# Optimization experiments

Measured on AMD Instinct MI355X. Metric: run time of the kernel, lower is better.

The kernel has to match this reference:

```python
import jax, jax.numpy as jnp
import numpy as np

B, D, C, H, L = 32768, 64, 64, 1024, 6
EPS = 1e-5
NIN = (D - D // 2) + C  # unchanged half + cond = 96
SPLIT = D // 2          # 32


def setup_inputs() -> dict:
    key = jax.random.key(0)
    ks = jax.random.split(key, 12)
    s = 0.05
    return {
        "z": jax.random.normal(ks[0], (B, D), jnp.float32),
        "cond": jax.random.normal(ks[1], (B, C), jnp.float32),
        "W1": jax.random.normal(ks[2], (L, NIN, H), jnp.float32) * s,
        "b1": jax.random.normal(ks[3], (L, H), jnp.float32) * s,
        "W2": jax.random.normal(ks[4], (L, H, H), jnp.float32) * s,
        "b2": jax.random.normal(ks[5], (L, H), jnp.float32) * s,
        "Ws": jax.random.normal(ks[6], (L, H, SPLIT), jnp.float32) * s,
        "bs": jax.random.normal(ks[7], (L, SPLIT), jnp.float32) * s,
        "Wt": jax.random.normal(ks[8], (L, H, SPLIT), jnp.float32) * s,
        "bt": jax.random.normal(ks[9], (L, SPLIT), jnp.float32) * s,
        "bn_w": 1.0 + 0.1 * jax.random.normal(ks[10], (L, D), jnp.float32),
        "bn_b": 0.1 * jax.random.normal(ks[11], (L, D), jnp.float32),
    }


def reference(z, cond, W1, b1, W2, b2, Ws, bs, Wt, bt, bn_w, bn_b):
    x = z
    log_det = jnp.zeros((z.shape[0],), z.dtype)
    for i in range(L):
        # 'even' mask keeps even indices on even layers, odd indices otherwise
        if i % 2 == 0:
            keep, chg = np.arange(0, D, 2), np.arange(1, D, 2)
        else:
            keep, chg = np.arange(1, D, 2), np.arange(0, D, 2)
        # 2-layer MLP on [x_keep, cond]
        h = jax.nn.relu(jnp.concatenate([x[:, keep], cond], axis=1) @ W1[i] + b1[i])
        h = jax.nn.relu(h @ W2[i] + b2[i])
        log_s = jnp.tanh(h @ Ws[i] + bs[i])          # (B, SPLIT)
        t = h @ Wt[i] + bt[i]                         # (B, SPLIT)
        x2t = x[:, chg] * jnp.exp(log_s) + t
        x = jnp.zeros_like(x).at[:, keep].set(x[:, keep]).at[:, chg].set(x2t)
        log_det = log_det + log_s.sum(axis=1)
        # BatchNorm1d, training mode: batch mean / biased variance, eps=1e-5
        mean = x.mean(axis=0)
        var = x.var(axis=0)
        x = (x - mean) * jax.lax.rsqrt(var + EPS) * bn_w[i] + bn_b[i]
        log_det = log_det + jnp.log(jnp.abs(bn_w[i])).sum()
    return x, log_det
```

## Files before the change

kernel.cpp:

```cpp
#include <hip/hip_runtime.h>
#include <math.h>

#define BB 32768
#define DD 64
#define CC 64
#define HH 1024
#define LL 6
#define SPLIT 32
#define NIN 96
#define EPSV 1e-5f

typedef short short8 __attribute__((ext_vector_type(8)));
typedef float f32x4 __attribute__((ext_vector_type(4)));
typedef unsigned short u16;

__device__ __forceinline__ u16 f2bf(float f) {
    union { float f; unsigned int u; } c; c.f = f;
    unsigned int u = c.u + 0x7FFFu + ((c.u >> 16) & 1u);
    return (u16)(u >> 16);
}

__device__ __forceinline__ void gl_lds16(const u16* g, u16* l) {
    __builtin_amdgcn_global_load_lds(
        (const __attribute__((address_space(1))) unsigned int*)g,
        (__attribute__((address_space(3))) unsigned int*)l, 16, 0, 0);
}

__global__ void transpose_cvt_kernel(const float* __restrict__ src, u16* __restrict__ dst,
                                     int R, int C, int Rpad,
                                     long long sstride, long long dstride)
{
    __shared__ float tile[32][33];
    const float* s = src + (size_t)blockIdx.z * sstride;
    u16* d = dst + (size_t)blockIdx.z * dstride;
    int r0 = blockIdx.x * 32, c0 = blockIdx.y * 32;
    int tc = threadIdx.x & 31, tr = threadIdx.x >> 5;
#pragma unroll
    for (int i = 0; i < 4; ++i) {
        int r = r0 + tr + i * 8;
        tile[tr + i * 8][tc] = (r < R) ? s[(size_t)r * C + c0 + tc] : 0.f;
    }
    __syncthreads();
#pragma unroll
    for (int i = 0; i < 4; ++i) {
        int cc = tr + i * 8;
        d[(size_t)(c0 + cc) * Rpad + r0 + tc] = f2bf(tile[tc][cc]);
    }
}

__global__ __launch_bounds__(256)
void init_ain_cond_kernel(const float* __restrict__ cond, u16* __restrict__ Ain)
{
    int t = blockIdx.x * 256 + threadIdx.x;
    int c = t % 96, r = t / 96;
    Ain[(size_t)r * 128 + 32 + c] = (c < CC) ? f2bf(cond[(size_t)r * CC + c]) : (u16)0;
}

__global__ __launch_bounds__(256)
void build_keep_kernel(const float* __restrict__ x, u16* __restrict__ Ain, int keep_off)
{
    int t = blockIdx.x * 256 + threadIdx.x;
    int c = t & 31, r = t >> 5;
    Ain[(size_t)r * 128 + c] = f2bf(x[(size_t)r * DD + 2 * c + keep_off]);
}

__global__ __launch_bounds__(512, 4)
void gemm_tiled(const u16* __restrict__ A,
                const u16* __restrict__ Bt,
                const float* __restrict__ bias,
                u16* __restrict__ Cc,
                int K)
{
    __shared__ u16 sA[2][8 * 512];
    __shared__ u16 sB[2][16 * 512];

    const int t = threadIdx.x;
    const int w = t >> 6, lane = t & 63;
    const int lane16 = lane & 15, quad = lane >> 4;
    const int wm = w >> 2, wn = w & 3;

    int id = blockIdx.x;
    int nby = gridDim.x >> 2;
    int xcd = id & 7, slot = id >> 3;
    int bx = slot & 3, byq = slot >> 2;
    int by = xcd * (nby >> 3) + byq;
    const int bm = by * 128, bn = bx * 256;

    const int niter = K >> 5;

    auto stage = [&](int it, int buf) {
        int k0 = it * 32;
#pragma unroll
        for (int e3 = 0; e3 < 3; ++e3) {
            int e = w + e3 * 8;
            if (e < 8) {
                const u16* g = A + (size_t)(bm + e * 16 + lane16) * K + k0 + quad * 8;
                gl_lds16(g, &sA[buf][e * 512]);
            } else {
                int j = e - 8;
                const u16* g = Bt + (size_t)(bn + j * 16 + lane16) * K + k0 + quad * 8;
                gl_lds16(g, &sB[buf][j * 512]);
            }
        }
    };

    f32x4 acc[4][4];
#pragma unroll
    for (int a = 0; a < 4; ++a)
#pragma unroll
        for (int b = 0; b < 4; ++b) acc[a][b] = (f32x4){0.f, 0.f, 0.f, 0.f};

    stage(0, 0);
    for (int it = 0; it < niter; ++it) {
        const int buf = it & 1;
        __syncthreads();
        if (it + 1 < niter) stage(it + 1, buf ^ 1);
        short8 af[4], bf[4];
#pragma unroll
        for (int a = 0; a < 4; ++a)
            af[a] = *(const short8*)(&sA[buf][(wm * 4 + a) * 512 + lane * 8]);
#pragma unroll
        for (int b = 0; b < 4; ++b)
            bf[b] = *(const short8*)(&sB[buf][(wn * 4 + b) * 512 + lane * 8]);
#pragma unroll
        for (int a = 0; a < 4; ++a)
#pragma unroll
            for (int b = 0; b < 4; ++b)
                acc[a][b] = __builtin_amdgcn_mfma_f32_16x16x32_bf16(af[a], bf[b], acc[a][b], 0, 0, 0);
    }
    __syncthreads();

    constexpr int ES = 72;
    float bv[4];
#pragma unroll
    for (int b = 0; b < 4; ++b) bv[b] = bias[bn + wn * 64 + b * 16 + lane16];
    u16* scr = ((u16*)sB) + w * (16 * ES);
#pragma unroll
    for (int a = 0; a < 4; ++a) {
#pragma unroll
        for (int b = 0; b < 4; ++b)
#pragma unroll
            for (int r = 0; r < 4; ++r) {
                float v = fmaxf(acc[a][b][r] + bv[b], 0.f);
                scr[(quad * 4 + r) * ES + b * 16 + lane16] = f2bf(v);
            }
#pragma unroll
        for (int ch = 0; ch < 2; ++ch) {
            int row = ch * 8 + (lane >> 3), colc = (lane & 7) * 8;
            short8 v = *(const short8*)(scr + row * ES + colc);
            *(short8*)(Cc + (size_t)(bm + wm * 64 + a * 16 + row) * 1024 + bn + wn * 64 + colc) = v;
        }
    }
}

__global__ __launch_bounds__(512)
void gemm3_coupling(const u16* __restrict__ A,
                    const u16* __restrict__ Bt,
                    const float* __restrict__ bs, const float* __restrict__ bt,
                    float* __restrict__ x, float* __restrict__ log_det,
                    float* __restrict__ stat_sum, float* __restrict__ stat_sumsq,
                    int keep_off, int row0)
{
    constexpr int ST_STRIDE = 66;
    __shared__ u16 stg[2][24 * 512];
    __shared__ float ssum[8][64], ssum2[8][64];
    float* sst = (float*)stg;

    const int t = threadIdx.x;
    const int w = t >> 6, lane = t & 63;
    const int lane16 = lane & 15, quad = lane >> 4;
    const int wm = w >> 1, wn = w & 1;
    const int bm = blockIdx.x * 128;

    auto stage = [&](int it, int buf) {
        int k0 = it * 64;
#pragma unroll
        for (int p = 0; p < 3; ++p) {
            int e = w + p * 8;
            if (e < 16) {
                int s = e >> 3, i = e & 7;
                const u16* g = A + (size_t)(bm + i * 16 + lane16) * HH + (k0 + s * 32 + quad * 8);
                gl_lds16(g, &stg[buf][e * 512]);
            } else {
                int j2 = e - 16, s = j2 >> 2, j = j2 & 3;
                const u16* g = Bt + (size_t)(j * 16 + lane16) * HH + (k0 + s * 32 + quad * 8);
                gl_lds16(g, &stg[buf][e * 512]);
            }
        }
    };

    f32x4 acc[2][2];
#pragma unroll
    for (int a = 0; a < 2; ++a)
#pragma unroll
        for (int b = 0; b < 2; ++b) acc[a][b] = (f32x4){0.f, 0.f, 0.f, 0.f};

    stage(0, 0);
    for (int it = 0; it < 16; ++it) {
        const int buf = it & 1;
        __syncthreads();
        if (it + 1 < 16) stage(it + 1, buf ^ 1);
        u16* ldsA = stg[buf];
        u16* ldsB = stg[buf] + 16 * 512;
#pragma unroll
        for (int s = 0; s < 2; ++s) {
            short8 af[2], bfr[2];
#pragma unroll
            for (int a = 0; a < 2; ++a)
                af[a] = *(const short8*)(ldsA + ((s * 8 + wm * 2 + a) * 512) + lane * 8);
#pragma unroll
            for (int b = 0; b < 2; ++b)
                bfr[b] = *(const short8*)(ldsB + ((s * 4 + wn * 2 + b) * 512) + lane * 8);
#pragma unroll
            for (int a = 0; a < 2; ++a)
#pragma unroll
                for (int b = 0; b < 2; ++b)
                    acc[a][b] = __builtin_amdgcn_mfma_f32_16x16x32_bf16(af[a], bfr[b], acc[a][b], 0, 0, 0);
        }
    }
    __syncthreads();

#pragma unroll
    for (int a = 0; a < 2; ++a)
#pragma unroll
        for (int b = 0; b < 2; ++b)
#pragma unroll
            for (int r = 0; r < 4; ++r) {
                int row = wm * 32 + a * 16 + quad * 4 + r;
                int col = wn * 32 + b * 16 + lane16;
                sst[row * ST_STRIDE + col] = acc[a][b][r];
            }
    __syncthreads();

    const int f = lane;
    const bool is_chg = ((f & 1) != keep_off);
    const int j = f >> 1;
    float bsj = 0.f, btj = 0.f;
    if (is_chg) { bsj = bs[j]; btj = bt[j]; }

    float lsum = 0.f, lsum2 = 0.f;
    for (int i = 0; i < 16; ++i) {
        int crow = w * 16 + i;
        int grow = row0 + bm + crow;
        float xv = x[(size_t)grow * DD + f];
        float ld = 0.f;
        if (is_chg) {
            float s_raw = sst[crow * ST_STRIDE + j];
            float t_raw = sst[crow * ST_STRIDE + SPLIT + j];
            float ls = tanhf(s_raw + bsj);
            float tv = t_raw + btj;
            xv = xv * expf(ls) + tv;
            x[(size_t)grow * DD + f] = xv;
            ld = ls;
        }
        for (int off = 32; off > 0; off >>= 1) ld += __shfl_down(ld, off, 64);
        if (f == 0) log_det[grow] += ld;
        lsum  += xv;
        lsum2 += xv * xv;
    }

    ssum[w][f]  = lsum;
    ssum2[w][f] = lsum2;
    __syncthreads();
    if (t < 64) {
        float a = 0.f, b = 0.f;
#pragma unroll
        for (int g = 0; g < 8; ++g) { a += ssum[g][t]; b += ssum2[g][t]; }
        atomicAdd(stat_sum + t, a);
        atomicAdd(stat_sumsq + t, b);
    }
}

__global__ __launch_bounds__(256)
void normalize_kernel(const float* __restrict__ xin, float* __restrict__ xout,
                      const float* __restrict__ stat_sum, const float* __restrict__ stat_sumsq,
                      const float* __restrict__ bn_w, const float* __restrict__ bn_b,
                      float* __restrict__ log_det,
                      u16* __restrict__ Ain, int off_next)
{
    __shared__ float sscale[64], sshift[64], scsum;
    int t = threadIdx.x;
    if (t < 64) {
        const float invB = 1.f / (float)BB;
        float mean = stat_sum[t] * invB;
        float var  = stat_sumsq[t] * invB - mean * mean;
        float inv  = rsqrtf(var + EPSV);
        float wv   = bn_w[t];
        float sc   = inv * wv;
        sscale[t] = sc;
        sshift[t] = bn_b[t] - mean * sc;
        float lg = logf(fabsf(wv));
        for (int off = 32; off > 0; off >>= 1) lg += __shfl_down(lg, off, 64);
        if (t == 0) scsum = lg;
    }
    __syncthreads();

    int idx = blockIdx.x * blockDim.x + t;
    int f0 = (idx & 15) * 4;
    int row = idx >> 4;
    float4 v = ((const float4*)xin)[idx];
    v.x = v.x * sscale[f0 + 0] + sshift[f0 + 0];
    v.y = v.y * sscale[f0 + 1] + sshift[f0 + 1];
    v.z = v.z * sscale[f0 + 2] + sshift[f0 + 2];
    v.w = v.w * sscale[f0 + 3] + sshift[f0 + 3];
    ((float4*)xout)[idx] = v;
    if ((idx & 15) == 0) log_det[row] += scsum;
    if (Ain) {
        float a0 = off_next ? v.y : v.x;
        float a1 = off_next ? v.w : v.z;
        ushort2 u; u.x = f2bf(a0); u.y = f2bf(a1);
        *(ushort2*)(Ain + (size_t)row * 128 + (f0 >> 1)) = u;
    }
}

extern "C" void kernel_launch(void* const* d_in, const int* in_sizes, int n_in,
                              void* d_out, int out_size, void* d_ws, size_t ws_size,
                              hipStream_t stream)
{
    const float* z    = (const float*)d_in[0];
    const float* cond = (const float*)d_in[1];
    const float* W1   = (const float*)d_in[2];
    const float* b1   = (const float*)d_in[3];
    const float* W2   = (const float*)d_in[4];
    const float* b2   = (const float*)d_in[5];
    const float* Ws   = (const float*)d_in[6];
    const float* bs   = (const float*)d_in[7];
    const float* Wt   = (const float*)d_in[8];
    const float* bt   = (const float*)d_in[9];
    const float* bn_w = (const float*)d_in[10];
    const float* bn_b = (const float*)d_in[11];

    float* out_x  = (float*)d_out;
    float* out_ld = out_x + (size_t)BB * DD;

    char* p = (char*)d_ws;
    size_t used = 0;
    auto alloc = [&](size_t bytes) { void* q = p + used; used += (bytes + 255) & ~(size_t)255; return q; };

    float* xbuf = (float*)alloc((size_t)BB * DD * 4);
    u16*   w1t  = (u16*)alloc((size_t)LL * HH * 128 * 2);
    u16*   w2t  = (u16*)alloc((size_t)LL * HH * HH * 2);
    u16*   wstt = (u16*)alloc((size_t)LL * 64 * HH * 2);
    u16*   Ain  = (u16*)alloc((size_t)BB * 128 * 2);
    float* stat_sum   = (float*)alloc(64 * 4);
    float* stat_sumsq = (float*)alloc(64 * 4);

    int CH = BB;
    while (CH > 8192 && used + (size_t)CH * 4096 + 4096 > ws_size) CH >>= 1;
    u16* h1 = (u16*)alloc((size_t)CH * HH * 2);
    u16* h2 = (u16*)alloc((size_t)CH * HH * 2);

    hipMemcpyAsync(xbuf, z, (size_t)BB * DD * sizeof(float), hipMemcpyDeviceToDevice, stream);
    hipMemsetAsync(out_ld, 0, (size_t)BB * sizeof(float), stream);

    transpose_cvt_kernel<<<dim3(128/32, HH/32, LL), 256, 0, stream>>>(
        W1, w1t, NIN, HH, 128, (long long)NIN * HH, (long long)HH * 128);
    transpose_cvt_kernel<<<dim3(HH/32, HH/32, LL), 256, 0, stream>>>(
        W2, w2t, HH, HH, HH, (long long)HH * HH, (long long)HH * HH);
    transpose_cvt_kernel<<<dim3(HH/32, SPLIT/32, LL), 256, 0, stream>>>(
        Ws, wstt, HH, SPLIT, HH, (long long)HH * SPLIT, (long long)64 * HH);
    transpose_cvt_kernel<<<dim3(HH/32, SPLIT/32, LL), 256, 0, stream>>>(
        Wt, wstt + (size_t)SPLIT * HH, HH, SPLIT, HH, (long long)HH * SPLIT, (long long)64 * HH);

    init_ain_cond_kernel<<<BB * 96 / 256, 256, 0, stream>>>(cond, Ain);
    build_keep_kernel<<<BB * 32 / 256, 256, 0, stream>>>(xbuf, Ain, 0);

    for (int l = 0; l < LL; ++l) {
        const int off = l & 1;
        hipMemsetAsync(stat_sum, 0, 2 * 64 * sizeof(float), stream);

        for (int c = 0; c < BB / CH; ++c) {
            const int row0 = c * CH;

            gemm_tiled<<<(CH / 128) * 4, 512, 0, stream>>>(
                Ain + (size_t)row0 * 128, w1t + (size_t)l * HH * 128,
                b1 + (size_t)l * HH, h1, 128);

            gemm_tiled<<<(CH / 128) * 4, 512, 0, stream>>>(
                h1, w2t + (size_t)l * HH * HH,
                b2 + (size_t)l * HH, h2, HH);

            gemm3_coupling<<<CH / 128, 512, 0, stream>>>(
                h2, wstt + (size_t)l * 64 * HH,
                bs + (size_t)l * SPLIT, bt + (size_t)l * SPLIT,
                xbuf, out_ld, stat_sum, stat_sumsq, off, row0);
        }

        float* xout = (l == LL - 1) ? out_x : xbuf;
        u16* ain_next = (l < LL - 1) ? Ain : nullptr;
        normalize_kernel<<<(BB * DD / 4) / 256, 256, 0, stream>>>(
            xbuf, xout, stat_sum, stat_sumsq,
            bn_w + (size_t)l * DD, bn_b + (size_t)l * DD,
            out_ld, ain_next, (l + 1) & 1);
    }
}
```

Measured before the change: 1.090 ms.

## Triple-buffer GEMM LDS staging with explicit waitcnt and inline ds_read

Moves the tiled bf16 GEMM from double to triple LDS buffering, prefetching two K-steps ahead. It replaces the full __syncthreads with a partial vmcnt wait plus s_barrier, and issues ds_read_b128 through inline asm before the next prefetch. The aim is to hide global-to-LDS latency and cut barrier stalls in the MLP GEMMs. In exchange it uses 50% more LDS, which may lower occupancy under launch_bounds(512,4). The hand-tuned vmcnt count and the duplicate staging of the last tile are correctness risks.

```diff
diff --git a/kernel.cpp b/kernel.cpp
--- a/kernel.cpp
+++ b/kernel.cpp
@@ -71,8 +71,8 @@
                 u16* __restrict__ Cc,
                 int K)
 {
-    __shared__ u16 sA[2][8 * 512];
-    __shared__ u16 sB[2][16 * 512];
+    __shared__ u16 sA[3][8 * 512];
+    __shared__ u16 sB[3][16 * 512];
 
     const int t = threadIdx.x;
     const int w = t >> 6, lane = t & 63;
@@ -110,23 +110,46 @@
 #pragma unroll
         for (int b = 0; b < 4; ++b) acc[a][b] = (f32x4){0.f, 0.f, 0.f, 0.f};
 
+    const unsigned sAb = (unsigned)(size_t)(__attribute__((address_space(3))) u16*)&sA[0][0];
+    const unsigned sBb = (unsigned)(size_t)(__attribute__((address_space(3))) u16*)&sB[0][0];
+    const unsigned aoff = (unsigned)(wm * 4096 + lane * 16);
+    const unsigned boff = (unsigned)(wn * 4096 + lane * 16);
+
     stage(0, 0);
+    stage(1, 1);
+    int buf = 0, sbuf = 2;
     for (int it = 0; it < niter; ++it) {
-        const int buf = it & 1;
-        __syncthreads();
-        if (it + 1 < niter) stage(it + 1, buf ^ 1);
-        short8 af[4], bf[4];
+        asm volatile("s_waitcnt vmcnt(3)");
+        __builtin_amdgcn_s_barrier();
+
+        const unsigned aA = sAb + (unsigned)(buf * 8192)  + aoff;
+        const unsigned aB = sBb + (unsigned)(buf * 16384) + boff;
+        short8 af0, af1, af2, af3, bf0, bf1, bf2, bf3;
+        asm volatile("ds_read_b128 %0, %1 offset:0"    : "=v"(af0) : "v"(aA));
+        asm volatile("ds_read_b128 %0, %1 offset:1024" : "=v"(af1) : "v"(aA));
+        asm volatile("ds_read_b128 %0, %1 offset:2048" : "=v"(af2) : "v"(aA));
+        asm volatile("ds_read_b128 %0, %1 offset:3072" : "=v"(af3) : "v"(aA));
+        asm volatile("ds_read_b128 %0, %1 offset:0"    : "=v"(bf0) : "v"(aB));
+        asm volatile("ds_read_b128 %0, %1 offset:1024" : "=v"(bf1) : "v"(aB));
+        asm volatile("ds_read_b128 %0, %1 offset:2048" : "=v"(bf2) : "v"(aB));
+        asm volatile("ds_read_b128 %0, %1 offset:3072" : "=v"(bf3) : "v"(aB));
+
+        if (it + 2 < niter)        stage(it + 2, sbuf);
+        else if (it + 2 == niter)  stage(niter - 1, sbuf);
+
+        asm volatile("s_waitcnt lgkmcnt(0)");
+        __builtin_amdgcn_sched_barrier(0);
+
+        short8 af[4] = {af0, af1, af2, af3};
+        short8 bfr[4] = {bf0, bf1, bf2, bf3};
 #pragma unroll
         for (int a = 0; a < 4; ++a)
-            af[a] = *(const short8*)(&sA[buf][(wm * 4 + a) * 512 + lane * 8]);
-#pragma unroll
-        for (int b = 0; b < 4; ++b)
-            bf[b] = *(const short8*)(&sB[buf][(wn * 4 + b) * 512 + lane * 8]);
-#pragma unroll
-        for (int a = 0; a < 4; ++a)
 #pragma unroll
             for (int b = 0; b < 4; ++b)
-                acc[a][b] = __builtin_amdgcn_mfma_f32_16x16x32_bf16(af[a], bf[b], acc[a][b], 0, 0, 0);
+                acc[a][b] = __builtin_amdgcn_mfma_f32_16x16x32_bf16(af[a], bfr[b], acc[a][b], 0, 0, 0);
+
+        buf  = (buf  == 2) ? 0 : buf  + 1;
+        sbuf = (sbuf == 2) ? 0 : sbuf + 1;
     }
     __syncthreads();
 
```

Measured after the change: 1.088 ms. No clear change (-0.2%).
